# Kernel tuning notes

Measured on AMD Instinct MI355X. Metric: run time of the kernel, lower is better.

Reference implementation:

```python
import jax, jax.numpy as jnp
import numpy as np

B, N, C, H = 8, 4096, 384, 8
HD = C // H  # 48
KERNEL_EPS = 1e-3
EPS = 1e-8


def setup_inputs() -> dict:
    key = jax.random.key(0)
    k1, k2, k3, k4 = jax.random.split(key, 4)
    x = jax.random.normal(k1, (B, N, C), dtype=jnp.float32)
    Wqkv = jax.random.normal(k2, (3 * C, C), dtype=jnp.float32) * 0.02
    Wproj = jax.random.normal(k3, (C, C), dtype=jnp.float32) * 0.02
    bproj = jax.random.normal(k4, (C,), dtype=jnp.float32) * 0.02
    return {"x": x, "Wqkv": Wqkv, "Wproj": Wproj, "bproj": bproj}


def reference(x, Wqkv, Wproj, bproj):
    # qkv projection (no bias): (B,N,3C) -> (3,B,H,N,HD)
    qkv = jnp.einsum('bnc,dc->bnd', x, Wqkv).reshape(B, N, 3, H, HD)
    qkv = jnp.transpose(qkv, (2, 0, 3, 1, 4))
    q, k, v = qkv[0], qkv[1], qkv[2]

    # generalized_kernel with projection_matrix=None, kernel_fn=ReLU
    dn = HD ** (-0.25)  # data normalizer
    qp = jax.nn.relu(dn * q) + KERNEL_EPS  # (B,H,N,HD) feature map, m=HD
    kp = jax.nn.relu(dn * k) + KERNEL_EPS

    ks = kp.sum(axis=2)                              # (B,H,m)
    D = jnp.einsum('bhnm,bhm->bhn', qp, ks)          # (B,H,N)
    kptv = jnp.einsum('bhnd,bhnm->bhdm', v, kp)      # (B,H,HD,m)
    out = jnp.einsum('bhnm,bhdm->bhnd', qp, kptv) / (D[..., None] + EPS)

    # faithful to original: reshape (B,H,N,HD) -> (B,N,C) WITHOUT head transpose
    out = out.reshape(B, N, C)
    return jnp.einsum('bnc,dc->bnd', out, Wproj) + bproj
```

## Files before the change

### kernel.cpp

```cpp
#include <hip/hip_runtime.h>
#include <hip/hip_bf16.h>


typedef __attribute__((ext_vector_type(8))) short short8;
typedef __attribute__((ext_vector_type(4))) float floatx4;

#define MFMA(a, b, c) __builtin_amdgcn_mfma_f32_16x16x32_bf16((a), (b), (c), 0, 0, 0)

__device__ __forceinline__ unsigned short f2bf(float f) {
  union { float f; unsigned u; } x; x.f = f;
  unsigned r = x.u + 0x7FFFu + ((x.u >> 16) & 1u);
  return (unsigned short)(r >> 16);
}

__device__ __forceinline__ void cv4(const float* __restrict__ in, unsigned short* __restrict__ out, int i) {
  float4 v = *(const float4*)(in + i);
  uint2 o;
  o.x = (unsigned)f2bf(v.x) | ((unsigned)f2bf(v.y) << 16);
  o.y = (unsigned)f2bf(v.z) | ((unsigned)f2bf(v.w) << 16);
  *(uint2*)(out + i) = o;
}

__global__ void conv_all(const float* __restrict__ x, const float* __restrict__ wq,
                         const float* __restrict__ wp,
                         unsigned short* __restrict__ xb, unsigned short* __restrict__ wqb,
                         unsigned short* __restrict__ wpb, float* __restrict__ accD) {
  const int tid = blockIdx.x * blockDim.x + threadIdx.x;
  const int stride = gridDim.x * blockDim.x * 4;
  for (int i = tid * 4; i < 12582912; i += stride) cv4(x, xb, i);
  for (int i = tid * 4; i < 442368; i += stride) cv4(wq, wqb, i);
  for (int i = tid * 4; i < 147456; i += stride) cv4(wp, wpb, i);
  float4 z = {0.f, 0.f, 0.f, 0.f};
  for (int i = tid * 4; i < 196608; i += stride) *(float4*)(accD + i) = z;
}

template <int EPI>
__global__ __launch_bounds__(256, 2) void gemm_bt(
    const unsigned short* __restrict__ A,
    const unsigned short* __restrict__ Bt,
    void* __restrict__ Cout,
    const float* __restrict__ bias,
    int M, int N, int K, int ldc) {
  __shared__ unsigned short As[128 * 64];
  __shared__ unsigned short Bs[128 * 64];
  const int NT = N >> 7;
  const int cpx = gridDim.x >> 3;
  const int bid = (blockIdx.x & 7) * cpx + (blockIdx.x >> 3);
  const int bn = bid % NT;
  const int bm = bid / NT;
  const int tid = threadIdx.x;
  const int w = tid >> 6, lane = tid & 63;
  const int wm = w >> 1, wn = w & 1;
  const int l15 = lane & 15, l4 = lane >> 4;

  floatx4 zero = {0.f, 0.f, 0.f, 0.f};
  floatx4 acc[4][4];
#pragma unroll
  for (int i = 0; i < 4; ++i)
#pragma unroll
    for (int j = 0; j < 4; ++j) acc[i][j] = zero;

  const int li0 = (w * 4) * 64 + lane;
  const size_t Abase = (size_t)(bm * 128) * K;
  const size_t Bbase = (size_t)(bn * 128) * K;

  for (int k0 = 0; k0 < K; k0 += 64) {
#pragma unroll
    for (int i = 0; i < 4; ++i) {
      int li = li0 + i * 64;
      int row = li >> 3;
      int col = (li & 7) << 3;
      const unsigned short* gA = A + Abase + (size_t)row * K + k0 + col;
      const unsigned short* gB = Bt + Bbase + (size_t)row * K + k0 + col;
      __builtin_amdgcn_global_load_lds((const __attribute__((address_space(1))) void*)gA,
                                       (__attribute__((address_space(3))) void*)&As[(w * 4 + i) * 512],
                                       16, 0, 0);
      __builtin_amdgcn_global_load_lds((const __attribute__((address_space(1))) void*)gB,
                                       (__attribute__((address_space(3))) void*)&Bs[(w * 4 + i) * 512],
                                       16, 0, 0);
    }
    __syncthreads();
#pragma unroll
    for (int kk = 0; kk < 2; ++kk) {
      short8 a[4], b[4];
#pragma unroll
      for (int mf = 0; mf < 4; ++mf)
        a[mf] = *(const short8*)&As[(wm * 64 + mf * 16 + l15) * 64 + kk * 32 + l4 * 8];
#pragma unroll
      for (int nf = 0; nf < 4; ++nf)
        b[nf] = *(const short8*)&Bs[(wn * 64 + nf * 16 + l15) * 64 + kk * 32 + l4 * 8];
#pragma unroll
      for (int mf = 0; mf < 4; ++mf)
#pragma unroll
        for (int nf = 0; nf < 4; ++nf)
          acc[mf][nf] = MFMA(a[mf], b[nf], acc[mf][nf]);
    }
    __syncthreads();
  }

  const float DN = 0.3799178430f;
#pragma unroll
  for (int mf = 0; mf < 4; ++mf) {
#pragma unroll
    for (int nf = 0; nf < 4; ++nf) {
      int gm0 = bm * 128 + wm * 64 + mf * 16 + l4 * 4;
      int gn = bn * 128 + wn * 64 + nf * 16 + l15;
#pragma unroll
      for (int r = 0; r < 4; ++r) {
        float v = acc[mf][nf][r];
        size_t off = (size_t)(gm0 + r) * ldc + gn;
        if (EPI == 0) {
          if (gn < 768) v = fmaxf(v * DN, 0.f) + 1e-3f;
          ((unsigned short*)Cout)[off] = f2bf(v);
        } else {
          ((float*)Cout)[off] = v + bias[gn];
        }
      }
    }
  }
}

__global__ __launch_bounds__(256, 2) void attn_ksum(
    const unsigned short* __restrict__ qkv,
    float* __restrict__ accD) {
  const int bh = blockIdx.x >> 3, g = blockIdx.x & 7;
  const int b = bh >> 3, h = bh & 7;
  const int tid = threadIdx.x, w = tid >> 6, lane = tid & 63;
  const int l15 = lane & 15, l4 = lane >> 4;
  __shared__ unsigned short Kpt[48 * 136];
  __shared__ unsigned short Vt[48 * 136];
  __shared__ float red[64 * 48];

  floatx4 zero = {0.f, 0.f, 0.f, 0.f};
  floatx4 acc[4][3];
#pragma unroll
  for (int i = 0; i < 4; ++i)
#pragma unroll
    for (int j = 0; j < 3; ++j) acc[i][j] = zero;

  unsigned short ov = (l15 == 0) ? (unsigned short)0x3F80 : (unsigned short)0;
  short8 ones;
#pragma unroll
  for (int e = 0; e < 8; ++e) ones[e] = (short)ov;

  const size_t rowbase = (size_t)b * 4096;
  const int t = tid >> 1, hf = tid & 1;

  for (int c = 0; c < 4; ++c) {
    int tok0 = g * 512 + c * 128;
    const unsigned short* kr = qkv + (rowbase + tok0 + t) * 1152 + 384 + h * 48 + hf * 24;
    const unsigned short* vr = kr + 384;
#pragma unroll
    for (int j = 0; j < 3; ++j) {
      short8 kv = *(const short8*)(kr + j * 8);
      short8 vv = *(const short8*)(vr + j * 8);
#pragma unroll
      for (int e = 0; e < 8; ++e) {
        int m = hf * 24 + j * 8 + e;
        Kpt[m * 136 + t] = (unsigned short)kv[e];
        Vt[m * 136 + t] = (unsigned short)vv[e];
      }
    }
    __syncthreads();
    {
      int col = w * 32 + l4 * 8;
      short8 a[3], bb[3];
#pragma unroll
      for (int f = 0; f < 3; ++f) {
        a[f] = *(const short8*)&Vt[(f * 16 + l15) * 136 + col];
        bb[f] = *(const short8*)&Kpt[(f * 16 + l15) * 136 + col];
      }
#pragma unroll
      for (int af = 0; af < 3; ++af)
#pragma unroll
        for (int bf = 0; bf < 3; ++bf)
          acc[af][bf] = MFMA(a[af], bb[bf], acc[af][bf]);
#pragma unroll
      for (int bf = 0; bf < 3; ++bf)
        acc[3][bf] = MFMA(ones, bb[bf], acc[3][bf]);
    }
    __syncthreads();
  }

  for (int i = tid; i < 64 * 48; i += 256) red[i] = 0.f;
  __syncthreads();
#pragma unroll
  for (int af = 0; af < 4; ++af)
#pragma unroll
    for (int bf = 0; bf < 3; ++bf)
#pragma unroll
      for (int r = 0; r < 4; ++r)
        atomicAdd(&red[(af * 16 + l4 * 4 + r) * 48 + bf * 16 + l15], acc[af][bf][r]);
  __syncthreads();
  float* dst = accD + (size_t)bh * 64 * 48;
  for (int i = tid; i < 64 * 48; i += 256) atomicAdd(&dst[i], red[i]);
}

__global__ __launch_bounds__(256, 2) void attn_out(
    const unsigned short* __restrict__ qkv,
    const float* __restrict__ accD,
    unsigned short* __restrict__ outr) {
  const int bh = blockIdx.x >> 4, tg = blockIdx.x & 15;
  const int b = bh >> 3, h = bh & 7;
  const int tid = threadIdx.x, w = tid >> 6, lane = tid & 63;
  const int l15 = lane & 15, l4 = lane >> 4;
  const int t0 = tg * 256 + w * 64;

  short8 bfr[2][4];
#pragma unroll
  for (int kk = 0; kk < 2; ++kk) {
#pragma unroll
    for (int nf = 0; nf < 4; ++nf) {
      int row = nf * 16 + l15;
      int c0 = kk * 32 + l4 * 8;
      short8 f;
      if (kk == 1 && l4 >= 2) {
#pragma unroll
        for (int e = 0; e < 8; ++e) f[e] = 0;
      } else {
        const float* p = accD + (size_t)bh * 3072 + row * 48 + c0;
        float4 v0 = *(const float4*)p;
        float4 v1 = *(const float4*)(p + 4);
        f[0] = (short)f2bf(v0.x); f[1] = (short)f2bf(v0.y);
        f[2] = (short)f2bf(v0.z); f[3] = (short)f2bf(v0.w);
        f[4] = (short)f2bf(v1.x); f[5] = (short)f2bf(v1.y);
        f[6] = (short)f2bf(v1.z); f[7] = (short)f2bf(v1.w);
      }
      bfr[kk][nf] = f;
    }
  }

  floatx4 zero = {0.f, 0.f, 0.f, 0.f};
  floatx4 acc[4][4];
#pragma unroll
  for (int i = 0; i < 4; ++i)
#pragma unroll
    for (int j = 0; j < 4; ++j) acc[i][j] = zero;

  const size_t rb = (size_t)b * 4096;
#pragma unroll
  for (int mf = 0; mf < 4; ++mf) {
#pragma unroll
    for (int kk = 0; kk < 2; ++kk) {
      int tt = t0 + mf * 16 + l15;
      short8 a = *(const short8*)&qkv[(rb + tt) * 1152 + h * 48 + kk * 32 + l4 * 8];
#pragma unroll
      for (int nf = 0; nf < 4; ++nf)
        acc[mf][nf] = MFMA(a, bfr[kk][nf], acc[mf][nf]);
    }
  }

#pragma unroll
  for (int mf = 0; mf < 4; ++mf) {
    float den[4];
#pragma unroll
    for (int r = 0; r < 4; ++r)
      den[r] = __shfl(acc[mf][3][r], lane & 48, 64) + 1e-8f;
#pragma unroll
    for (int nf = 0; nf < 3; ++nf) {
#pragma unroll
      for (int r = 0; r < 4; ++r) {
        int tt = t0 + mf * 16 + l4 * 4 + r;
        int d = nf * 16 + l15;
        float v = acc[mf][nf][r] / den[r];
        int np = h * 512 + (tt >> 3);
        int cp = (tt & 7) * 48 + d;
        outr[(rb + np) * 384 + cp] = f2bf(v);
      }
    }
  }
}

extern "C" void kernel_launch(void* const* d_in, const int* in_sizes, int n_in,
                              void* d_out, int out_size, void* d_ws, size_t ws_size,
                              hipStream_t stream) {
  const float* x = (const float*)d_in[0];
  const float* Wqkv = (const float*)d_in[1];
  const float* Wproj = (const float*)d_in[2];
  const float* bproj = (const float*)d_in[3];

  char* ws = (char*)d_ws;
  unsigned short* xb = (unsigned short*)(ws);
  unsigned short* wqkvb = (unsigned short*)(ws + 25165824);
  unsigned short* wprojb = (unsigned short*)(ws + 26050560);
  unsigned short* qkvA = (unsigned short*)(ws + 26345472);
  float* accD = (float*)(ws + 101842944);
  unsigned short* outr = (unsigned short*)(ws + 102629376);

  conv_all<<<2048, 256, 0, stream>>>(x, Wqkv, Wproj, xb, wqkvb, wprojb, accD);
  gemm_bt<0><<<2304, 256, 0, stream>>>(xb, wqkvb, (void*)qkvA, nullptr, 32768, 1152, 384, 1152);
  attn_ksum<<<512, 256, 0, stream>>>(qkvA, accD);
  attn_out<<<1024, 256, 0, stream>>>(qkvA, accD, outr);
  gemm_bt<1><<<768, 256, 0, stream>>>(outr, wprojb, d_out, bproj, 32768, 384, 384, 384);
}
```

Before: 217.7 us.

## Write K and V transposed per head from QKV GEMM epilogue, simplify ksum

The QKV GEMM epilogue now writes Q as a compact row-major buffer and writes K and V in a per-(batch, head, feature) token-contiguous transposed layout. This lets the ksum kernel load MFMA operands straight from global memory, with no LDS transpose staging and no barriers. Launch bounds are also raised for the GEMM (3 blocks) and the ksum kernel (4 blocks). The trade-off is that the transposed epilogue stores are scattered 8-byte writes, and the higher occupancy targets may add register pressure.

```diff
diff --git a/kernel.cpp b/kernel.cpp
--- a/kernel.cpp
+++ b/kernel.cpp
@@ -35,10 +35,12 @@
 }
 
 template <int EPI>
-__global__ __launch_bounds__(256, 2) void gemm_bt(
+__global__ __launch_bounds__(256, 3) void gemm_bt(
     const unsigned short* __restrict__ A,
     const unsigned short* __restrict__ Bt,
     void* __restrict__ Cout,
+    unsigned short* __restrict__ Kt,
+    unsigned short* __restrict__ Vt,
     const float* __restrict__ bias,
     int M, int N, int K, int ldc) {
   __shared__ unsigned short As[128 * 64];
@@ -99,36 +101,71 @@
   }
 
   const float DN = 0.3799178430f;
-#pragma unroll
-  for (int mf = 0; mf < 4; ++mf) {
+  if (EPI == 1) {
+#pragma unroll
+    for (int mf = 0; mf < 4; ++mf) {
+#pragma unroll
+      for (int nf = 0; nf < 4; ++nf) {
+        int gm0 = bm * 128 + wm * 64 + mf * 16 + l4 * 4;
+        int gn = bn * 128 + wn * 64 + nf * 16 + l15;
+#pragma unroll
+        for (int r = 0; r < 4; ++r)
+          ((float*)Cout)[(size_t)(gm0 + r) * ldc + gn] = acc[mf][nf][r] + bias[gn];
+      }
+    }
+  } else if (bn < 3) {
+#pragma unroll
+    for (int mf = 0; mf < 4; ++mf) {
+#pragma unroll
+      for (int nf = 0; nf < 4; ++nf) {
+        int gm0 = bm * 128 + wm * 64 + mf * 16 + l4 * 4;
+        int gn = bn * 128 + wn * 64 + nf * 16 + l15;
+#pragma unroll
+        for (int r = 0; r < 4; ++r) {
+          float v = fmaxf(acc[mf][nf][r] * DN, 0.f) + 1e-3f;
+          ((unsigned short*)Cout)[(size_t)(gm0 + r) * 384 + gn] = f2bf(v);
+        }
+      }
+    }
+  } else {
+    const int isV = (bn >= 6);
+    unsigned short* T = isV ? Vt : Kt;
+    const int fbase = bn * 128 - (isV ? 768 : 384) + wn * 64;
+    const int b = (bm * 128) >> 12;
+    const int tokb = ((bm * 128) & 4095) + wm * 64;
 #pragma unroll
     for (int nf = 0; nf < 4; ++nf) {
-      int gm0 = bm * 128 + wm * 64 + mf * 16 + l4 * 4;
-      int gn = bn * 128 + wn * 64 + nf * 16 + l15;
-#pragma unroll
-      for (int r = 0; r < 4; ++r) {
-        float v = acc[mf][nf][r];
-        size_t off = (size_t)(gm0 + r) * ldc + gn;
-        if (EPI == 0) {
-          if (gn < 768) v = fmaxf(v * DN, 0.f) + 1e-3f;
-          ((unsigned short*)Cout)[off] = f2bf(v);
-        } else {
-          ((float*)Cout)[off] = v + bias[gn];
+      int fk = fbase + nf * 16 + l15;
+      int h = fk / 48;
+      int m = fk - h * 48;
+      unsigned short* dst = T + (((size_t)(b * 8 + h) * 48 + m) << 12);
+#pragma unroll
+      for (int mf = 0; mf < 4; ++mf) {
+        int tok = tokb + mf * 16 + l4 * 4;
+        float v0 = acc[mf][nf][0], v1 = acc[mf][nf][1];
+        float v2 = acc[mf][nf][2], v3 = acc[mf][nf][3];
+        if (!isV) {
+          v0 = fmaxf(v0 * DN, 0.f) + 1e-3f;
+          v1 = fmaxf(v1 * DN, 0.f) + 1e-3f;
+          v2 = fmaxf(v2 * DN, 0.f) + 1e-3f;
+          v3 = fmaxf(v3 * DN, 0.f) + 1e-3f;
         }
-      }
-    }
-  }
-}
-
-__global__ __launch_bounds__(256, 2) void attn_ksum(
-    const unsigned short* __restrict__ qkv,
+        uint2 o;
+        o.x = (unsigned)f2bf(v0) | ((unsigned)f2bf(v1) << 16);
+        o.y = (unsigned)f2bf(v2) | ((unsigned)f2bf(v3) << 16);
+        *(uint2*)(dst + tok) = o;
+      }
+    }
+  }
+}
+
+__global__ __launch_bounds__(256, 4) void attn_ksum(
+    const unsigned short* __restrict__ Kt,
+    const unsigned short* __restrict__ Vt,
     float* __restrict__ accD) {
   const int bh = blockIdx.x >> 3, g = blockIdx.x & 7;
-  const int b = bh >> 3, h = bh & 7;
   const int tid = threadIdx.x, w = tid >> 6, lane = tid & 63;
   const int l15 = lane & 15, l4 = lane >> 4;
-  __shared__ unsigned short Kpt[48 * 136];
-  __shared__ unsigned short Vt[48 * 136];
   __shared__ float red[64 * 48];
 
   floatx4 zero = {0.f, 0.f, 0.f, 0.f};
@@ -143,43 +180,26 @@
 #pragma unroll
   for (int e = 0; e < 8; ++e) ones[e] = (short)ov;
 
-  const size_t rowbase = (size_t)b * 4096;
-  const int t = tid >> 1, hf = tid & 1;
-
+  const size_t base = (size_t)bh * 48 * 4096;
+  const int tok0 = g * 512 + w * 128 + l4 * 8;
+
+#pragma unroll
   for (int c = 0; c < 4; ++c) {
-    int tok0 = g * 512 + c * 128;
-    const unsigned short* kr = qkv + (rowbase + tok0 + t) * 1152 + 384 + h * 48 + hf * 24;
-    const unsigned short* vr = kr + 384;
-#pragma unroll
-    for (int j = 0; j < 3; ++j) {
-      short8 kv = *(const short8*)(kr + j * 8);
-      short8 vv = *(const short8*)(vr + j * 8);
-#pragma unroll
-      for (int e = 0; e < 8; ++e) {
-        int m = hf * 24 + j * 8 + e;
-        Kpt[m * 136 + t] = (unsigned short)kv[e];
-        Vt[m * 136 + t] = (unsigned short)vv[e];
-      }
-    }
-    __syncthreads();
-    {
-      int col = w * 32 + l4 * 8;
-      short8 a[3], bb[3];
-#pragma unroll
-      for (int f = 0; f < 3; ++f) {
-        a[f] = *(const short8*)&Vt[(f * 16 + l15) * 136 + col];
-        bb[f] = *(const short8*)&Kpt[(f * 16 + l15) * 136 + col];
-      }
-#pragma unroll
-      for (int af = 0; af < 3; ++af)
-#pragma unroll
-        for (int bf = 0; bf < 3; ++bf)
-          acc[af][bf] = MFMA(a[af], bb[bf], acc[af][bf]);
+    int t0 = tok0 + c * 32;
+    short8 a[3], bb[3];
+#pragma unroll
+    for (int f = 0; f < 3; ++f) {
+      a[f] = *(const short8*)&Vt[base + (size_t)(f * 16 + l15) * 4096 + t0];
+      bb[f] = *(const short8*)&Kt[base + (size_t)(f * 16 + l15) * 4096 + t0];
+    }
+#pragma unroll
+    for (int af = 0; af < 3; ++af)
 #pragma unroll
       for (int bf = 0; bf < 3; ++bf)
-        acc[3][bf] = MFMA(ones, bb[bf], acc[3][bf]);
-    }
-    __syncthreads();
+        acc[af][bf] = MFMA(a[af], bb[bf], acc[af][bf]);
+#pragma unroll
+    for (int bf = 0; bf < 3; ++bf)
+      acc[3][bf] = MFMA(ones, bb[bf], acc[3][bf]);
   }
 
   for (int i = tid; i < 64 * 48; i += 256) red[i] = 0.f;
@@ -197,7 +217,7 @@
 }
 
 __global__ __launch_bounds__(256, 2) void attn_out(
-    const unsigned short* __restrict__ qkv,
+    const unsigned short* __restrict__ qp,
     const float* __restrict__ accD,
     unsigned short* __restrict__ outr) {
   const int bh = blockIdx.x >> 4, tg = blockIdx.x & 15;
@@ -243,7 +263,7 @@
 #pragma unroll
     for (int kk = 0; kk < 2; ++kk) {
       int tt = t0 + mf * 16 + l15;
-      short8 a = *(const short8*)&qkv[(rb + tt) * 1152 + h * 48 + kk * 32 + l4 * 8];
+      short8 a = *(const short8*)&qp[(rb + tt) * 384 + h * 48 + kk * 32 + l4 * 8];
 #pragma unroll
       for (int nf = 0; nf < 4; ++nf)
         acc[mf][nf] = MFMA(a, bfr[kk][nf], acc[mf][nf]);
@@ -283,13 +303,15 @@
   unsigned short* xb = (unsigned short*)(ws);
   unsigned short* wqkvb = (unsigned short*)(ws + 25165824);
   unsigned short* wprojb = (unsigned short*)(ws + 26050560);
-  unsigned short* qkvA = (unsigned short*)(ws + 26345472);
-  float* accD = (float*)(ws + 101842944);
-  unsigned short* outr = (unsigned short*)(ws + 102629376);
+  unsigned short* qp = (unsigned short*)(ws + 26345472);
+  unsigned short* Kt = (unsigned short*)(ws + 51511552);
+  unsigned short* Vt = (unsigned short*)(ws + 76677376);
+  float* accD = (float*)(ws + 101843200);
+  unsigned short* outr = (unsigned short*)(ws + 102629632);
 
   conv_all<<<2048, 256, 0, stream>>>(x, Wqkv, Wproj, xb, wqkvb, wprojb, accD);
-  gemm_bt<0><<<2304, 256, 0, stream>>>(xb, wqkvb, (void*)qkvA, nullptr, 32768, 1152, 384, 1152);
-  attn_ksum<<<512, 256, 0, stream>>>(qkvA, accD);
-  attn_out<<<1024, 256, 0, stream>>>(qkvA, accD, outr);
-  gemm_bt<1><<<768, 256, 0, stream>>>(outr, wprojb, d_out, bproj, 32768, 384, 384, 384);
-}
+  gemm_bt<0><<<2304, 256, 0, stream>>>(xb, wqkvb, (void*)qp, Kt, Vt, nullptr, 32768, 1152, 384, 384);
+  attn_ksum<<<512, 256, 0, stream>>>(Kt, Vt, accD);
+  attn_out<<<1024, 256, 0, stream>>>(qp, accD, outr);
+  gemm_bt<1><<<768, 256, 0, stream>>>(outr, wprojb, d_out, nullptr, nullptr, bproj, 32768, 384, 384, 384);
+}
```

Measured after the change: 224.0 us. +2.9%, slower.
